# Kernel tuning notes

Measured on AMD Instinct MI355X. Metric: run time of the kernel, lower is better.

Reference implementation:

```python
import jax, jax.numpy as jnp
import numpy as np

D_MODEL = 1024
B, T = 4, 2048
LN_EPS = 1e-5


def setup_inputs() -> dict:
    key = jax.random.key(0)
    ks = jax.random.split(key, 8)
    d = D_MODEL
    x = jax.random.normal(ks[0], (B, T, d), dtype=jnp.float32)
    # linear params (fan-in scaled)
    W_in = jax.random.normal(ks[1], (d, 4 * d), dtype=jnp.float32) / np.sqrt(d)
    b_in = jnp.zeros((4 * d,), dtype=jnp.float32)
    W_out = jax.random.normal(ks[2], (2 * d, d), dtype=jnp.float32) / np.sqrt(2 * d)
    b_out = jnp.zeros((d,), dtype=jnp.float32)
    # LRU initializer (matches the torch module's initializer())
    rng = np.random.default_rng(0)
    r_min, r_max = 0.9, 0.999
    u1 = rng.random(d)
    u2 = rng.random(d)
    nu_log = np.log(-0.5 * np.log(u1 * (r_max ** 2 - r_min ** 2) + r_min ** 2))
    theta_log = np.log(u2 * np.pi * 2)
    gamma_log = np.log(np.sqrt(1 - np.exp(-np.exp(nu_log)) ** 2))
    # LayerNorm affine params
    ln_w = jnp.ones((2 * d,), dtype=jnp.float32)
    ln_b = jnp.zeros((2 * d,), dtype=jnp.float32)
    return {
        "x": x,
        "W_in": W_in, "b_in": b_in,
        "nu_log": jnp.asarray(nu_log, dtype=jnp.float32),
        "theta_log": jnp.asarray(theta_log, dtype=jnp.float32),
        "gamma_log": jnp.asarray(gamma_log, dtype=jnp.float32),
        "ln_w": ln_w, "ln_b": ln_b,
        "W_out": W_out, "b_out": b_out,
    }


def _complex_scan(in_r, in_i, f_r, f_i):
    """h_t = f * h_{t-1} + in_t over axis=1, complex math in real/imag pairs."""
    def combine(l, r):
        a1r, a1i, b1r, b1i = l
        a2r, a2i, b2r, b2i = r
        ar = a2r * a1r - a2i * a1i
        ai = a2r * a1i + a2i * a1r
        br = a2r * b1r - a2i * b1i + b2r
        bi = a2r * b1i + a2i * b1r + b2i
        return (ar, ai, br, bi)
    fr = jnp.broadcast_to(f_r, in_r.shape)
    fi = jnp.broadcast_to(f_i, in_i.shape)
    _, _, hr, hi = jax.lax.associative_scan(combine, (fr, fi, in_r, in_i), axis=1)
    return hr, hi


def reference(x, W_in, b_in, nu_log, theta_log, gamma_log, ln_w, ln_b, W_out, b_out):
    d = x.shape[-1]
    u = x @ W_in + b_in                       # [B, T, 4d]
    v, o = u[..., :2 * d], u[..., 2 * d:]     # each [B, T, 2d]
    nu = jnp.exp(-jnp.exp(nu_log))            # [d]
    theta = jnp.exp(theta_log)
    gamma = jnpp_exp = jnp.exp(gamma_log)
    f_r = nu * jnp.cos(theta)
    f_i = nu * jnp.sin(theta)
    in_r = gamma * v[..., :d]                 # [B, T, d]
    in_i = gamma * v[..., d:]
    h_r, h_i = _complex_scan(in_r, in_i, f_r, f_i)
    y = jnp.concatenate([h_r, h_i], axis=-1) * jax.nn.silu(o)  # [B, T, 2d]
    mu = jnp.mean(y, axis=-1, keepdims=True)
    var = jnp.mean(jnp.square(y - mu), axis=-1, keepdims=True)
    y = (y - mu) * jax.lax.rsqrt(var + LN_EPS) * ln_w + ln_b
    return y @ W_out + b_out                  # [B, T, d]
```

## Files before the change

### kernel.cpp

```cpp
#include <hip/hip_runtime.h>
#include <hip/hip_bf16.h>

#define D_MODEL 1024
#define BB 4
#define TT 2048
#define ROWS (BB*TT)
#define NCHUNK 64
#define CHLEN 32

typedef __attribute__((ext_vector_type(8))) short short8;
typedef __attribute__((ext_vector_type(4))) float floatx4;

static __device__ __forceinline__ ushort f2bf(float f) {
    union { float f; unsigned u; } v; v.f = f;
    unsigned r = v.u + 0x7FFF + ((v.u >> 16) & 1);
    return (ushort)(r >> 16);
}
static __device__ __forceinline__ float bf2f(ushort b) {
    union { unsigned u; float f; } v; v.u = ((unsigned)b) << 16;
    return v.f;
}

#define GLOAD_LDS16(gp, lp)                                                 \
    __builtin_amdgcn_global_load_lds(                                       \
        (const __attribute__((address_space(1))) void*)(gp),                \
        (__attribute__((address_space(3))) void*)(lp), 16, 0, 0)

#define PREP_A 8192
#define PREP_B 4096
#define PREP_C 2048
__global__ __launch_bounds__(256) void prep_all(
    const float* __restrict__ x, ushort* __restrict__ xb,
    const float* __restrict__ W_in, ushort* __restrict__ WinT,
    const float* __restrict__ W_out, ushort* __restrict__ W1T,
    const float* __restrict__ lnw, const float* __restrict__ lnb,
    float* __restrict__ s1, float* __restrict__ c2,
    const float* __restrict__ nu_log, const float* __restrict__ theta_log,
    const float* __restrict__ gamma_log,
    float* __restrict__ fr, float* __restrict__ fi, float* __restrict__ gm) {
    __shared__ float smem[32 * 33 + 8 * 32 * 2];
    int bid = blockIdx.x, tid = threadIdx.x;
    if (bid < PREP_A) {
        int i = bid * 256 + tid;
        float4 v = ((const float4*)x)[i];
        ushort4 o;
        o.x = f2bf(v.x); o.y = f2bf(v.y); o.z = f2bf(v.z); o.w = f2bf(v.w);
        ((ushort4*)xb)[i] = o;
    } else if (bid < PREP_A + PREP_B) {
        int b2 = bid - PREP_A;
        int n0 = (b2 & 127) * 32, k0 = (b2 >> 7) * 32;
        int tx = tid & 31, ty = tid >> 5;
        float (*tile)[33] = (float (*)[33])smem;
#pragma unroll
        for (int j = 0; j < 4; ++j)
            tile[ty + j*8][tx] = W_in[(size_t)(k0 + ty + j*8) * 4096 + n0 + tx];
        __syncthreads();
#pragma unroll
        for (int j = 0; j < 4; ++j)
            WinT[(size_t)(n0 + ty + j*8) * 1024 + k0 + tx] = f2bf(tile[tx][ty + j*8]);
    } else if (bid < PREP_A + PREP_B + PREP_C) {
        int b2 = bid - PREP_A - PREP_B;
        int n0 = (b2 & 31) * 32, k0 = (b2 >> 5) * 32;
        int tx = tid & 31, ty = tid >> 5;
        float (*tile)[33] = (float (*)[33])smem;
        float* red1 = smem + 32 * 33;
        float* red2 = red1 + 8 * 32;
        float p1 = 0.f, p2 = 0.f;
#pragma unroll
        for (int j = 0; j < 4; ++j) {
            int k = k0 + ty + j * 8;
            float w = W_out[(size_t)k * 1024 + n0 + tx];
            float lw = lnw[k], lb = lnb[k];
            tile[ty + j*8][tx] = lw * w;
            p1 += lw * w; p2 += lb * w;
        }
        __syncthreads();
#pragma unroll
        for (int j = 0; j < 4; ++j)
            W1T[(size_t)(n0 + ty + j*8) * 2048 + k0 + tx] = f2bf(tile[tx][ty + j*8]);
        red1[ty * 32 + tx] = p1; red2[ty * 32 + tx] = p2;
        __syncthreads();
        if (ty == 0) {
            float a = 0.f, b = 0.f;
#pragma unroll
            for (int t = 0; t < 8; ++t) { a += red1[t * 32 + tx]; b += red2[t * 32 + tx]; }
            atomicAdd(&s1[n0 + tx], a);
            atomicAdd(&c2[n0 + tx], b);
        }
    } else {
        int c = (bid - PREP_A - PREP_B - PREP_C) * 256 + tid;
        if (c < D_MODEL) {
            float nu = expf(-expf(nu_log[c]));
            float th = expf(theta_log[c]);
            fr[c] = nu * cosf(th);
            fi[c] = nu * sinf(th);
            gm[c] = expf(gamma_log[c]);
        }
    }
}

#define P_PRE  do { __builtin_amdgcn_sched_barrier(0); __builtin_amdgcn_s_barrier();  \
                    asm volatile("s_waitcnt lgkmcnt(0)" ::: "memory");                \
                    __builtin_amdgcn_sched_barrier(0);                                \
                    __builtin_amdgcn_s_setprio(1); } while (0)
#define P_POST do { __builtin_amdgcn_s_setprio(0); __builtin_amdgcn_sched_barrier(0); \
                    __builtin_amdgcn_s_barrier();                                     \
                    __builtin_amdgcn_sched_barrier(0); } while (0)

__global__ __launch_bounds__(512) void gemm256(
    const ushort* __restrict__ A, const ushort* __restrict__ B,
    int K, const float* __restrict__ bias,
    const float* __restrict__ gamma,
    ushort* __restrict__ out_r, ushort* __restrict__ out_i,
    ushort* __restrict__ out_o) {
    __shared__ ushort LA[2][256 * 64];
    __shared__ ushort LB[2][256 * 64];
    int tid = threadIdx.x;
    int lane = tid & 63;
    int wave = tid >> 6;
    int wp = wave >> 2;
    int wq = wave & 3;
    int lr = lane & 15, q = lane >> 4;
    int swl = lr & 7;
    int rs8 = tid >> 3, ch = tid & 7;
    int sw8 = (ch ^ (rs8 & 7)) * 8;

    int gx = gridDim.x;
    int nwg = gx * gridDim.y;
    int lid = blockIdx.y * gx + blockIdx.x;
    int per = nwg >> 3;
    int sid = (lid & 7) * per + (lid >> 3);
    long m0 = (long)(sid / gx) * 256;
    long n0 = (long)(sid % gx) * 256;
    const int NT = K >> 6;

    const ushort* Abase = A + (size_t)(m0 + rs8) * K + sw8;
    const ushort* Bbase = B + (size_t)(n0 + rs8) * K + sw8;

    floatx4 acc[8][4] = {};

#define STG_A(kt, P, R) GLOAD_LDS16(Abase + (size_t)(R) * K + (kt), \
                                    &LA[P][((R) + rs8) * 64 + ch * 8])
#define STG_B(kt, P, R) GLOAD_LDS16(Bbase + (size_t)(R) * K + (kt), \
                                    &LB[P][((R) + rs8) * 64 + ch * 8])

    STG_A(0, 0, 0);    STG_A(0, 0, 64);
    STG_B(0, 0, 0);    STG_B(0, 0, 64);
    STG_B(0, 0, 128);  STG_B(0, 0, 192);
    STG_A(0, 0, 128);  STG_A(0, 0, 192);
    STG_A(64, 1, 0);   STG_A(64, 1, 64);
    STG_B(64, 1, 0);   STG_B(64, 1, 64);
    STG_B(64, 1, 128); STG_B(64, 1, 192);
    asm volatile("s_waitcnt vmcnt(6)" ::: "memory");
    __builtin_amdgcn_s_barrier();

    for (int t = 0; t < NT; ++t) {
        const int p = t & 1;
        int kt1 = (t + 1 < NT) ? (t + 1) << 6 : 0;
        int kt2 = (t + 2 < NT) ? (t + 2) << 6 : 0;
        short8 a[2][4], b0[2][2], b1[2][2];

#pragma unroll
        for (int ks = 0; ks < 2; ++ks) {
#pragma unroll
            for (int r = 0; r < 4; ++r)
                a[ks][r] = *(const short8*)&LA[p][(wp * 64 + r * 16 + lr) * 64 + ((ks * 4 + q) ^ swl) * 8];
#pragma unroll
            for (int c = 0; c < 2; ++c)
                b0[ks][c] = *(const short8*)&LB[p][(wq * 32 + c * 16 + lr) * 64 + ((ks * 4 + q) ^ swl) * 8];
        }
        STG_A(kt1, p ^ 1, 128); STG_A(kt1, p ^ 1, 192);
        P_PRE;
#pragma unroll
        for (int ks = 0; ks < 2; ++ks)
#pragma unroll
            for (int r = 0; r < 4; ++r)
#pragma unroll
                for (int c = 0; c < 2; ++c)
                    acc[r][c] = __builtin_amdgcn_mfma_f32_16x16x32_bf16(
                        a[ks][r], b0[ks][c], acc[r][c], 0, 0, 0);
        P_POST;

#pragma unroll
        for (int ks = 0; ks < 2; ++ks)
#pragma unroll
            for (int c = 0; c < 2; ++c)
                b1[ks][c] = *(const short8*)&LB[p][(128 + wq * 32 + c * 16 + lr) * 64 + ((ks * 4 + q) ^ swl) * 8];
        STG_A(kt2, p, 0); STG_A(kt2, p, 64);
        P_PRE;
#pragma unroll
        for (int ks = 0; ks < 2; ++ks)
#pragma unroll
            for (int r = 0; r < 4; ++r)
#pragma unroll
                for (int c = 0; c < 2; ++c)
                    acc[r][2 + c] = __builtin_amdgcn_mfma_f32_16x16x32_bf16(
                        a[ks][r], b1[ks][c], acc[r][2 + c], 0, 0, 0);
        P_POST;

#pragma unroll
        for (int ks = 0; ks < 2; ++ks)
#pragma unroll
            for (int r = 0; r < 4; ++r)
                a[ks][r] = *(const short8*)&LA[p][(128 + wp * 64 + r * 16 + lr) * 64 + ((ks * 4 + q) ^ swl) * 8];
        STG_B(kt2, p, 0); STG_B(kt2, p, 64);
        P_PRE;
#pragma unroll
        for (int ks = 0; ks < 2; ++ks)
#pragma unroll
            for (int r = 0; r < 4; ++r)
#pragma unroll
                for (int c = 0; c < 2; ++c)
                    acc[4 + r][c] = __builtin_amdgcn_mfma_f32_16x16x32_bf16(
                        a[ks][r], b0[ks][c], acc[4 + r][c], 0, 0, 0);
        P_POST;

        STG_B(kt2, p, 128); STG_B(kt2, p, 192);
        asm volatile("s_waitcnt vmcnt(6)" ::: "memory");
        P_PRE;
#pragma unroll
        for (int ks = 0; ks < 2; ++ks)
#pragma unroll
            for (int r = 0; r < 4; ++r)
#pragma unroll
                for (int c = 0; c < 2; ++c)
                    acc[4 + r][2 + c] = __builtin_amdgcn_mfma_f32_16x16x32_bf16(
                        a[ks][r], b1[ks][c], acc[4 + r][2 + c], 0, 0, 0);
        P_POST;
    }
    asm volatile("s_waitcnt vmcnt(0)" ::: "memory");

    int sector = (int)(n0 >> 10);
    if (sector < 2) {
        ushort* dst = sector ? out_i : out_r;
#pragma unroll
        for (int nh = 0; nh < 2; ++nh)
#pragma unroll
            for (int c = 0; c < 2; ++c) {
                int lc = (int)(n0 & 1023) + nh * 128 + wq * 32 + c * 16 + lr;
                float bv = bias[(sector << 10) + lc];
                float gv = gamma[lc];
#pragma unroll
                for (int mh = 0; mh < 2; ++mh)
#pragma unroll
                    for (int r = 0; r < 4; ++r)
#pragma unroll
                        for (int g = 0; g < 4; ++g) {
                            long row = m0 + mh * 128 + wp * 64 + r * 16 + q * 4 + g;
                            dst[row * 1024 + lc] = f2bf(gv * (acc[mh * 4 + r][nh * 2 + c][g] + bv));
                        }
            }
    } else {
        int oc0 = (int)(n0 - 2048);
#pragma unroll
        for (int nh = 0; nh < 2; ++nh)
#pragma unroll
            for (int c = 0; c < 2; ++c) {
                int oc = oc0 + nh * 128 + wq * 32 + c * 16 + lr;
                float bv = bias[2048 + oc];
#pragma unroll
                for (int mh = 0; mh < 2; ++mh)
#pragma unroll
                    for (int r = 0; r < 4; ++r)
#pragma unroll
                        for (int g = 0; g < 4; ++g) {
                            long row = m0 + mh * 128 + wp * 64 + r * 16 + q * 4 + g;
                            out_o[row * 2048 + oc] = f2bf(acc[mh * 4 + r][nh * 2 + c][g] + bv);
                        }
            }
    }
#undef STG_A
#undef STG_B
}

__global__ __launch_bounds__(512) void gemm2_8ph(
    const ushort* __restrict__ A, const ushort* __restrict__ B,
    int K, int N, const float* __restrict__ bias, float* __restrict__ outC,
    const float* __restrict__ mu, const float* __restrict__ rs,
    const float* __restrict__ s1, const float* __restrict__ c2) {
    __shared__ ushort LA[2][128 * 64];
    __shared__ ushort LB[2][256 * 64];
    int tid = threadIdx.x;
    int lane = tid & 63;
    int wave = tid >> 6;
    int wp = wave >> 2;
    int wq = wave & 3;
    int lr = lane & 15, q = lane >> 4;
    int swl = lr & 7;
    int rs8 = tid >> 3, ch = tid & 7;
    int sw8 = (ch ^ (rs8 & 7)) * 8;

    int gx = gridDim.x;
    int nwg = gx * gridDim.y;
    int lid = blockIdx.y * gx + blockIdx.x;
    int per = nwg >> 3;
    int sid = (lid & 7) * per + (lid >> 3);
    long m0 = (long)(sid / gx) * 128;
    long n0 = (long)(sid % gx) * 256;
    const int NT = K >> 6;

    const ushort* Abase = A + (size_t)(m0 + rs8) * K + sw8;
    const ushort* Bbase = B + (size_t)(n0 + rs8) * K + sw8;

    floatx4 acc[4][4] = {};

#define STG2_A(kt, P, R) GLOAD_LDS16(Abase + (size_t)(R) * K + (kt), \
                                     &LA[P][((R) + rs8) * 64 + ch * 8])
#define STG2_B(kt, P, R) GLOAD_LDS16(Bbase + (size_t)(R) * K + (kt), \
                                     &LB[P][((R) + rs8) * 64 + ch * 8])

    STG2_A(0, 0, 0);   STG2_A(0, 0, 64);
    STG2_B(0, 0, 0);   STG2_B(0, 0, 64);
    STG2_B(0, 0, 128); STG2_B(0, 0, 192);
    STG2_A(64, 1, 0);
    STG2_B(64, 1, 0);  STG2_B(64, 1, 64);
    asm volatile("s_waitcnt vmcnt(3)" ::: "memory");
    __builtin_amdgcn_s_barrier();

    for (int t = 0; t < NT; ++t) {
        const int p = t & 1;
        int kt1 = (t + 1 < NT) ? (t + 1) << 6 : 0;
        int kt2 = (t + 2 < NT) ? (t + 2) << 6 : 0;
        short8 a[2][2], b0[2][2], b1[2][2];

#pragma unroll
        for (int ks = 0; ks < 2; ++ks) {
#pragma unroll
            for (int r = 0; r < 2; ++r)
                a[ks][r] = *(const short8*)&LA[p][(wp * 32 + r * 16 + lr) * 64 + ((ks * 4 + q) ^ swl) * 8];
#pragma unroll
            for (int c = 0; c < 2; ++c)
                b0[ks][c] = *(const short8*)&LB[p][(wq * 32 + c * 16 + lr) * 64 + ((ks * 4 + q) ^ swl) * 8];
        }
        STG2_A(kt1, p ^ 1, 64);
        STG2_B(kt1, p ^ 1, 128); STG2_B(kt1, p ^ 1, 192);
        P_PRE;
#pragma unroll
        for (int ks = 0; ks < 2; ++ks)
#pragma unroll
            for (int r = 0; r < 2; ++r)
#pragma unroll
                for (int c = 0; c < 2; ++c)
                    acc[r][c] = __builtin_amdgcn_mfma_f32_16x16x32_bf16(
                        a[ks][r], b0[ks][c], acc[r][c], 0, 0, 0);
        P_POST;

#pragma unroll
        for (int ks = 0; ks < 2; ++ks)
#pragma unroll
            for (int c = 0; c < 2; ++c)
                b1[ks][c] = *(const short8*)&LB[p][(128 + wq * 32 + c * 16 + lr) * 64 + ((ks * 4 + q) ^ swl) * 8];
        P_PRE;
#pragma unroll
        for (int ks = 0; ks < 2; ++ks)
#pragma unroll
            for (int r = 0; r < 2; ++r)
#pragma unroll
                for (int c = 0; c < 2; ++c)
                    acc[r][2 + c] = __builtin_amdgcn_mfma_f32_16x16x32_bf16(
                        a[ks][r], b1[ks][c], acc[r][2 + c], 0, 0, 0);
        P_POST;

#pragma unroll
        for (int ks = 0; ks < 2; ++ks)
#pragma unroll
            for (int r = 0; r < 2; ++r)
                a[ks][r] = *(const short8*)&LA[p][(64 + wp * 32 + r * 16 + lr) * 64 + ((ks * 4 + q) ^ swl) * 8];
        STG2_A(kt2, p, 0);
        P_PRE;
#pragma unroll
        for (int ks = 0; ks < 2; ++ks)
#pragma unroll
            for (int r = 0; r < 2; ++r)
#pragma unroll
                for (int c = 0; c < 2; ++c)
                    acc[2 + r][c] = __builtin_amdgcn_mfma_f32_16x16x32_bf16(
                        a[ks][r], b0[ks][c], acc[2 + r][c], 0, 0, 0);
        P_POST;

        STG2_B(kt2, p, 0); STG2_B(kt2, p, 64);
        asm volatile("s_waitcnt vmcnt(3)" ::: "memory");
        P_PRE;
#pragma unroll
        for (int ks = 0; ks < 2; ++ks)
#pragma unroll
            for (int r = 0; r < 2; ++r)
#pragma unroll
                for (int c = 0; c < 2; ++c)
                    acc[2 + r][2 + c] = __builtin_amdgcn_mfma_f32_16x16x32_bf16(
                        a[ks][r], b1[ks][c], acc[2 + r][2 + c], 0, 0, 0);
        P_POST;
    }
    asm volatile("s_waitcnt vmcnt(0)" ::: "memory");

#pragma unroll
    for (int nh = 0; nh < 2; ++nh)
#pragma unroll
        for (int c = 0; c < 2; ++c) {
            long col = n0 + nh * 128 + wq * 32 + c * 16 + lr;
            float bc = c2[col] + bias[col];
            float s1c = s1[col];
#pragma unroll
            for (int mh = 0; mh < 2; ++mh)
#pragma unroll
                for (int r = 0; r < 2; ++r)
#pragma unroll
                    for (int g = 0; g < 4; ++g) {
                        long row = m0 + mh * 64 + wp * 32 + r * 16 + q * 4 + g;
                        outC[row * (long)N + col] =
                            rs[row] * (acc[mh * 2 + r][nh * 2 + c][g] - mu[row] * s1c) + bc;
                    }
        }
#undef STG2_A
#undef STG2_B
}

__global__ __launch_bounds__(256) void scan_carries(
    const ushort* __restrict__ in_r, const ushort* __restrict__ in_i,
    float* __restrict__ carry,
    const float* __restrict__ fr_, const float* __restrict__ fi_) {
    int t = blockIdx.x * 256 + threadIdx.x;
    int cp = t & 511;
    int ck = (t >> 9) & (NCHUNK - 1);
    int b = t >> 15;
    int c0 = cp * 2;
    float f0r = fr_[c0], f0i = fi_[c0], f1r = fr_[c0 + 1], f1i = fi_[c0 + 1];
    size_t base = ((size_t)(b * TT + ck * CHLEN)) * 1024 + c0;
    float h0r = 0.f, h0i = 0.f, h1r = 0.f, h1i = 0.f;
#pragma unroll 8
    for (int j = 0; j < CHLEN; ++j) {
        uint ur = *(const uint*)(in_r + base + (size_t)j * 1024);
        uint ui = *(const uint*)(in_i + base + (size_t)j * 1024);
        float r0 = bf2f((ushort)ur), r1 = bf2f((ushort)(ur >> 16));
        float i0 = bf2f((ushort)ui), i1 = bf2f((ushort)(ui >> 16));
        float n0r = f0r * h0r - f0i * h0i + r0;
        float n0i = f0r * h0i + f0i * h0r + i0;
        float n1r = f1r * h1r - f1i * h1i + r1;
        float n1i = f1r * h1i + f1i * h1r + i1;
        h0r = n0r; h0i = n0i; h1r = n1r; h1i = n1i;
    }
    ((float4*)carry)[((size_t)b * NCHUNK + ck) * 512 + cp] =
        make_float4(h0r, h0i, h1r, h1i);
}

__global__ __launch_bounds__(256) void carry_prefix(
    float* __restrict__ carry,
    const float* __restrict__ fr_, const float* __restrict__ fi_) {
    int t = blockIdx.x * 256 + threadIdx.x;
    int cp = t & 511, b = t >> 9;
    int c0 = cp * 2;
    float a0r = fr_[c0], a0i = fi_[c0], a1r = fr_[c0 + 1], a1i = fi_[c0 + 1];
#pragma unroll
    for (int s = 0; s < 5; ++s) {
        float t0r = a0r * a0r - a0i * a0i, t0i = 2.f * a0r * a0i;
        float t1r = a1r * a1r - a1i * a1i, t1i = 2.f * a1r * a1i;
        a0r = t0r; a0i = t0i; a1r = t1r; a1i = t1i;
    }
    float4* base = (float4*)carry + (size_t)b * NCHUNK * 512 + cp;
    float C0r = 0.f, C0i = 0.f, C1r = 0.f, C1i = 0.f;
    for (int k = 0; k < NCHUNK; ++k) {
        float4 s = base[(size_t)k * 512];
        base[(size_t)k * 512] = make_float4(C0r, C0i, C1r, C1i);
        float n0r = a0r * C0r - a0i * C0i + s.x;
        float n0i = a0r * C0i + a0i * C0r + s.y;
        float n1r = a1r * C1r - a1i * C1i + s.z;
        float n1i = a1r * C1i + a1i * C1r + s.w;
        C0r = n0r; C0i = n0i; C1r = n1r; C1i = n1i;
    }
}

__global__ __launch_bounds__(256) void scan_apply(
    const ushort* __restrict__ in_r, const ushort* __restrict__ in_i,
    const float* __restrict__ carry,
    const float* __restrict__ fr_, const float* __restrict__ fi_,
    const ushort* __restrict__ o, ushort* __restrict__ yb) {
    int t = blockIdx.x * 256 + threadIdx.x;
    int cp = t & 511;
    int ck = (t >> 9) & (NCHUNK - 1);
    int b = t >> 15;
    int c0 = cp * 2;
    float f0r = fr_[c0], f0i = fi_[c0], f1r = fr_[c0 + 1], f1i = fi_[c0 + 1];
    float4 C = ((const float4*)carry)[((size_t)b * NCHUNK + ck) * 512 + cp];
    float h0r = C.x, h0i = C.y, h1r = C.z, h1i = C.w;
    size_t base = ((size_t)(b * TT + ck * CHLEN)) * 1024 + c0;
    size_t rowbase = (size_t)(b * TT + ck * CHLEN);
#pragma unroll 4
    for (int j = 0; j < CHLEN; ++j) {
        uint ur = *(const uint*)(in_r + base + (size_t)j * 1024);
        uint ui = *(const uint*)(in_i + base + (size_t)j * 1024);
        size_t ob = (rowbase + j) * 2048 + c0;
        uint uo1 = *(const uint*)(o + ob);
        uint uo2 = *(const uint*)(o + ob + 1024);
        float r0 = bf2f((ushort)ur), r1 = bf2f((ushort)(ur >> 16));
        float i0 = bf2f((ushort)ui), i1 = bf2f((ushort)(ui >> 16));
        float n0r = f0r * h0r - f0i * h0i + r0;
        float n0i = f0r * h0i + f0i * h0r + i0;
        float n1r = f1r * h1r - f1i * h1i + r1;
        float n1i = f1r * h1i + f1i * h1r + i1;
        h0r = n0r; h0i = n0i; h1r = n1r; h1i = n1i;
        float o00 = bf2f((ushort)uo1), o01 = bf2f((ushort)(uo1 >> 16));
        float o10 = bf2f((ushort)uo2), o11 = bf2f((ushort)(uo2 >> 16));
        float y00 = h0r * o00 / (1.f + __expf(-o00));
        float y01 = h1r * o01 / (1.f + __expf(-o01));
        float y10 = h0i * o10 / (1.f + __expf(-o10));
        float y11 = h1i * o11 / (1.f + __expf(-o11));
        *(uint*)(yb + ob) = (uint)f2bf(y00) | ((uint)f2bf(y01) << 16);
        *(uint*)(yb + ob + 1024) = (uint)f2bf(y10) | ((uint)f2bf(y11) << 16);
    }
}

__global__ __launch_bounds__(256) void row_stats(
    const ushort* __restrict__ yb, float* __restrict__ mu_o,
    float* __restrict__ rs_o) {
    long row = blockIdx.x;
    int tid = threadIdx.x;
    const ushort* p = yb + row * 2048 + tid * 8;
    uint4 raw = *(const uint4*)p;
    float s = 0.f, s2 = 0.f;
    unsigned w[4] = {raw.x, raw.y, raw.z, raw.w};
#pragma unroll
    for (int j = 0; j < 4; ++j) {
        float a = bf2f((ushort)(w[j] & 0xffff));
        float b = bf2f((ushort)(w[j] >> 16));
        s += a + b; s2 += a * a + b * b;
    }
#pragma unroll
    for (int off = 32; off > 0; off >>= 1) {
        s += __shfl_down(s, off, 64);
        s2 += __shfl_down(s2, off, 64);
    }
    __shared__ float red[8];
    int wv = tid >> 6;
    if ((tid & 63) == 0) { red[wv] = s; red[4 + wv] = s2; }
    __syncthreads();
    if (tid == 0) {
        s = red[0] + red[1] + red[2] + red[3];
        s2 = red[4] + red[5] + red[6] + red[7];
        float mu = s * (1.f / 2048.f);
        float var = s2 * (1.f / 2048.f) - mu * mu;
        mu_o[row] = mu;
        rs_o[row] = rsqrtf(var + 1e-5f);
    }
}


extern "C" void kernel_launch(void* const* d_in, const int* in_sizes, int n_in,
                              void* d_out, int out_size, void* d_ws, size_t ws_size,
                              hipStream_t stream) {
    const float* x         = (const float*)d_in[0];
    const float* W_in      = (const float*)d_in[1];
    const float* b_in      = (const float*)d_in[2];
    const float* nu_log    = (const float*)d_in[3];
    const float* theta_log = (const float*)d_in[4];
    const float* gamma_log = (const float*)d_in[5];
    const float* ln_w      = (const float*)d_in[6];
    const float* ln_b      = (const float*)d_in[7];
    const float* W_out     = (const float*)d_in[8];
    const float* b_out     = (const float*)d_in[9];
    float* out = (float*)d_out;

    char* ws = (char*)d_ws;
    size_t off = 0;
    auto alloc = [&](size_t bytes) {
        char* p = ws + off;
        off += (bytes + 255) & ~(size_t)255;
        return p;
    };
    ushort* xb    = (ushort*)alloc((size_t)ROWS * 1024 * 2);
    ushort* WinT  = (ushort*)alloc((size_t)4096 * 1024 * 2);
    ushort* W1T   = (ushort*)alloc((size_t)1024 * 2048 * 2);
    float*  fr    = (float*)alloc(1024 * 4);
    float*  fi    = (float*)alloc(1024 * 4);
    float*  gm    = (float*)alloc(1024 * 4);
    float*  s1c2  = (float*)alloc(2048 * 4);
    float*  s1    = s1c2;
    float*  c2    = s1c2 + 1024;
    ushort* in_r  = (ushort*)alloc((size_t)ROWS * 1024 * 2);
    ushort* in_i  = (ushort*)alloc((size_t)ROWS * 1024 * 2);
    ushort* obuf  = (ushort*)alloc((size_t)ROWS * 2048 * 2);
    float*  carry = (float*)alloc((size_t)BB * 1024 * NCHUNK * 2 * 4);
    ushort* yb    = (ushort*)alloc((size_t)ROWS * 2048 * 2);
    float*  muv   = (float*)alloc(ROWS * 4);
    float*  rsv   = (float*)alloc(ROWS * 4);

    hipMemsetAsync(s1c2, 0, 2048 * 4, stream);

    prep_all<<<PREP_A + PREP_B + PREP_C + 4, 256, 0, stream>>>(
        x, xb, W_in, WinT, W_out, W1T, ln_w, ln_b, s1, c2,
        nu_log, theta_log, gamma_log, fr, fi, gm);

    gemm256<<<dim3(4096 / 256, ROWS / 256), 512, 0, stream>>>(
        xb, WinT, 1024, b_in, gm, in_r, in_i, obuf);

    scan_carries<<<BB * 512 * NCHUNK / 256, 256, 0, stream>>>(in_r, in_i, carry, fr, fi);
    carry_prefix<<<BB * 512 / 256, 256, 0, stream>>>(carry, fr, fi);
    scan_apply<<<BB * 512 * NCHUNK / 256, 256, 0, stream>>>(
        in_r, in_i, carry, fr, fi, obuf, yb);

    row_stats<<<ROWS, 256, 0, stream>>>(yb, muv, rsv);

    gemm2_8ph<<<dim3(1024 / 256, ROWS / 128), 512, 0, stream>>>(
        yb, W1T, 2048, 1024, b_out, out, muv, rsv, s1, c2);
}
```

Measured before the change: 273.8 us.

## Fuse carry prefix and row statistics into the scan apply kernel

Removes the separate carry_prefix and row_stats kernels. Each scan_apply2 block, one per (batch, chunk), recomputes its own carry prefix by serially combining all preceding chunk carries, then computes the per-row LayerNorm mean and rstd with wave shuffles and a shared-memory reduction while producing y. This saves two launches and a full re-read of yb, at the cost of redundant carry work in later chunks and a cross-wave reduction on every timestep.

```diff
diff --git a/kernel.cpp b/kernel.cpp
--- a/kernel.cpp
+++ b/kernel.cpp
@@ -443,45 +443,38 @@
         make_float4(h0r, h0i, h1r, h1i);
 }
 
-__global__ __launch_bounds__(256) void carry_prefix(
-    float* __restrict__ carry,
-    const float* __restrict__ fr_, const float* __restrict__ fi_) {
-    int t = blockIdx.x * 256 + threadIdx.x;
-    int cp = t & 511, b = t >> 9;
+__global__ __launch_bounds__(512) void scan_apply2(
+    const ushort* __restrict__ in_r, const ushort* __restrict__ in_i,
+    const float* __restrict__ carry,
+    const float* __restrict__ fr_, const float* __restrict__ fi_,
+    const ushort* __restrict__ o, ushort* __restrict__ yb,
+    float* __restrict__ mu_o, float* __restrict__ rs_o) {
+    int bid = blockIdx.x;
+    int b = bid >> 6, ck = bid & (NCHUNK - 1);
+    int cp = threadIdx.x;
+    int wave = cp >> 6, lane = cp & 63;
     int c0 = cp * 2;
-    float a0r = fr_[c0], a0i = fi_[c0], a1r = fr_[c0 + 1], a1i = fi_[c0 + 1];
+    float f0r = fr_[c0], f0i = fi_[c0], f1r = fr_[c0 + 1], f1i = fi_[c0 + 1];
+
+    float a0r = f0r, a0i = f0i, a1r = f1r, a1i = f1i;
 #pragma unroll
     for (int s = 0; s < 5; ++s) {
         float t0r = a0r * a0r - a0i * a0i, t0i = 2.f * a0r * a0i;
         float t1r = a1r * a1r - a1i * a1i, t1i = 2.f * a1r * a1i;
         a0r = t0r; a0i = t0i; a1r = t1r; a1i = t1i;
     }
-    float4* base = (float4*)carry + (size_t)b * NCHUNK * 512 + cp;
-    float C0r = 0.f, C0i = 0.f, C1r = 0.f, C1i = 0.f;
-    for (int k = 0; k < NCHUNK; ++k) {
-        float4 s = base[(size_t)k * 512];
-        base[(size_t)k * 512] = make_float4(C0r, C0i, C1r, C1i);
-        float n0r = a0r * C0r - a0i * C0i + s.x;
-        float n0i = a0r * C0i + a0i * C0r + s.y;
-        float n1r = a1r * C1r - a1i * C1i + s.z;
-        float n1i = a1r * C1i + a1i * C1r + s.w;
-        C0r = n0r; C0i = n0i; C1r = n1r; C1i = n1i;
-    }
-}
-
-__global__ __launch_bounds__(256) void scan_apply(
-    const ushort* __restrict__ in_r, const ushort* __restrict__ in_i,
-    const float* __restrict__ carry,
-    const float* __restrict__ fr_, const float* __restrict__ fi_,
-    const ushort* __restrict__ o, ushort* __restrict__ yb) {
-    int t = blockIdx.x * 256 + threadIdx.x;
-    int cp = t & 511;
-    int ck = (t >> 9) & (NCHUNK - 1);
-    int b = t >> 15;
-    int c0 = cp * 2;
-    float f0r = fr_[c0], f0i = fi_[c0], f1r = fr_[c0 + 1], f1i = fi_[c0 + 1];
-    float4 C = ((const float4*)carry)[((size_t)b * NCHUNK + ck) * 512 + cp];
-    float h0r = C.x, h0i = C.y, h1r = C.z, h1i = C.w;
+    const float4* cb = (const float4*)carry + (size_t)b * NCHUNK * 512 + cp;
+    float h0r = 0.f, h0i = 0.f, h1r = 0.f, h1i = 0.f;
+    for (int k = 0; k < ck; ++k) {
+        float4 s = cb[(size_t)k * 512];
+        float n0r = a0r * h0r - a0i * h0i + s.x;
+        float n0i = a0r * h0i + a0i * h0r + s.y;
+        float n1r = a1r * h1r - a1i * h1i + s.z;
+        float n1i = a1r * h1i + a1i * h1r + s.w;
+        h0r = n0r; h0i = n0i; h1r = n1r; h1i = n1i;
+    }
+
+    __shared__ float sred[2][8][CHLEN];
     size_t base = ((size_t)(b * TT + ck * CHLEN)) * 1024 + c0;
     size_t rowbase = (size_t)(b * TT + ck * CHLEN);
 #pragma unroll 4
@@ -506,40 +499,24 @@
         float y11 = h1i * o11 / (1.f + __expf(-o11));
         *(uint*)(yb + ob) = (uint)f2bf(y00) | ((uint)f2bf(y01) << 16);
         *(uint*)(yb + ob + 1024) = (uint)f2bf(y10) | ((uint)f2bf(y11) << 16);
-    }
-}
-
-__global__ __launch_bounds__(256) void row_stats(
-    const ushort* __restrict__ yb, float* __restrict__ mu_o,
-    float* __restrict__ rs_o) {
-    long row = blockIdx.x;
-    int tid = threadIdx.x;
-    const ushort* p = yb + row * 2048 + tid * 8;
-    uint4 raw = *(const uint4*)p;
-    float s = 0.f, s2 = 0.f;
-    unsigned w[4] = {raw.x, raw.y, raw.z, raw.w};
-#pragma unroll
-    for (int j = 0; j < 4; ++j) {
-        float a = bf2f((ushort)(w[j] & 0xffff));
-        float b = bf2f((ushort)(w[j] >> 16));
-        s += a + b; s2 += a * a + b * b;
-    }
-#pragma unroll
-    for (int off = 32; off > 0; off >>= 1) {
-        s += __shfl_down(s, off, 64);
-        s2 += __shfl_down(s2, off, 64);
-    }
-    __shared__ float red[8];
-    int wv = tid >> 6;
-    if ((tid & 63) == 0) { red[wv] = s; red[4 + wv] = s2; }
+        float sp = y00 + y01 + y10 + y11;
+        float s2p = y00 * y00 + y01 * y01 + y10 * y10 + y11 * y11;
+#pragma unroll
+        for (int off = 32; off > 0; off >>= 1) {
+            sp += __shfl_xor(sp, off, 64);
+            s2p += __shfl_xor(s2p, off, 64);
+        }
+        if (lane == 0) { sred[0][wave][j] = sp; sred[1][wave][j] = s2p; }
+    }
     __syncthreads();
-    if (tid == 0) {
-        s = red[0] + red[1] + red[2] + red[3];
-        s2 = red[4] + red[5] + red[6] + red[7];
+    if (cp < CHLEN) {
+        float s = 0.f, s2 = 0.f;
+#pragma unroll
+        for (int w = 0; w < 8; ++w) { s += sred[0][w][cp]; s2 += sred[1][w][cp]; }
         float mu = s * (1.f / 2048.f);
         float var = s2 * (1.f / 2048.f) - mu * mu;
-        mu_o[row] = mu;
-        rs_o[row] = rsqrtf(var + 1e-5f);
+        mu_o[rowbase + cp] = mu;
+        rs_o[rowbase + cp] = rsqrtf(var + 1e-5f);
     }
 }
 
@@ -578,7 +555,7 @@
     ushort* in_r  = (ushort*)alloc((size_t)ROWS * 1024 * 2);
     ushort* in_i  = (ushort*)alloc((size_t)ROWS * 1024 * 2);
     ushort* obuf  = (ushort*)alloc((size_t)ROWS * 2048 * 2);
-    float*  carry = (float*)alloc((size_t)BB * 1024 * NCHUNK * 2 * 4);
+    float*  carry = (float*)alloc((size_t)BB * 512 * NCHUNK * 4 * 4);
     ushort* yb    = (ushort*)alloc((size_t)ROWS * 2048 * 2);
     float*  muv   = (float*)alloc(ROWS * 4);
     float*  rsv   = (float*)alloc(ROWS * 4);
@@ -593,11 +570,9 @@
         xb, WinT, 1024, b_in, gm, in_r, in_i, obuf);
 
     scan_carries<<<BB * 512 * NCHUNK / 256, 256, 0, stream>>>(in_r, in_i, carry, fr, fi);
-    carry_prefix<<<BB * 512 / 256, 256, 0, stream>>>(carry, fr, fi);
-    scan_apply<<<BB * 512 * NCHUNK / 256, 256, 0, stream>>>(
-        in_r, in_i, carry, fr, fi, obuf, yb);
-
-    row_stats<<<ROWS, 256, 0, stream>>>(yb, muv, rsv);
+
+    scan_apply2<<<BB * NCHUNK, 512, 0, stream>>>(
+        in_r, in_i, carry, fr, fi, obuf, yb, muv, rsv);
 
     gemm2_8ph<<<dim3(1024 / 256, ROWS / 128), 512, 0, stream>>>(
         yb, W1T, 2048, 1024, b_out, out, muv, rsv, s1, c2);
```

After: 284.3 us. +3.9%, slower.

## Restructure second GEMM main loop into a two-tile double-buffered schedule

Applied to the files above, without the earlier changes.

Replaces the 8-phase fine-grained interleaved prefetch schedule in the output GEMM with a simpler scheme. Each iteration now handles two K-tiles, and whole tiles are staged into the alternate LDS buffer while the current one is consumed. All B fragments are loaded up front and the global loads are fully drained with vmcnt(0) at each half-step. This cuts scheduling complexity, but the prefetch distance drops to one tile and the wait is full, so load latency may be less hidden than before. It also raises register pressure from holding b0 and b1 together.

```diff
diff --git a/kernel.cpp b/kernel.cpp
--- a/kernel.cpp
+++ b/kernel.cpp
@@ -273,7 +273,7 @@
 #undef STG_B
 }
 
-__global__ __launch_bounds__(512) void gemm2_8ph(
+__global__ __launch_bounds__(512) void gemm2_2t(
     const ushort* __restrict__ A, const ushort* __restrict__ B,
     int K, int N, const float* __restrict__ bias, float* __restrict__ outC,
     const float* __restrict__ mu, const float* __restrict__ rs,
@@ -298,6 +298,7 @@
     long m0 = (long)(sid / gx) * 128;
     long n0 = (long)(sid % gx) * 256;
     const int NT = K >> 6;
+    const int NI = NT >> 1;
 
     const ushort* Abase = A + (size_t)(m0 + rs8) * K + sw8;
     const ushort* Bbase = B + (size_t)(n0 + rs8) * K + sw8;
@@ -308,87 +309,110 @@
                                      &LA[P][((R) + rs8) * 64 + ch * 8])
 #define STG2_B(kt, P, R) GLOAD_LDS16(Bbase + (size_t)(R) * K + (kt), \
                                      &LB[P][((R) + rs8) * 64 + ch * 8])
-
-    STG2_A(0, 0, 0);   STG2_A(0, 0, 64);
-    STG2_B(0, 0, 0);   STG2_B(0, 0, 64);
-    STG2_B(0, 0, 128); STG2_B(0, 0, 192);
-    STG2_A(64, 1, 0);
-    STG2_B(64, 1, 0);  STG2_B(64, 1, 64);
-    asm volatile("s_waitcnt vmcnt(3)" ::: "memory");
+#define STG2_TILE(kt, P) do { STG2_A(kt, P, 0); STG2_A(kt, P, 64);            \
+                              STG2_B(kt, P, 0); STG2_B(kt, P, 64);            \
+                              STG2_B(kt, P, 128); STG2_B(kt, P, 192); } while (0)
+
+    STG2_TILE(0, 0);
+    asm volatile("s_waitcnt vmcnt(0)" ::: "memory");
     __builtin_amdgcn_s_barrier();
 
-    for (int t = 0; t < NT; ++t) {
-        const int p = t & 1;
-        int kt1 = (t + 1 < NT) ? (t + 1) << 6 : 0;
-        int kt2 = (t + 2 < NT) ? (t + 2) << 6 : 0;
+    for (int i = 0; i < NI; ++i) {
+        int t0 = 2 * i;
+        int kt1 = (t0 + 1) << 6;
+        int kt2 = (t0 + 2 < NT) ? (t0 + 2) << 6 : 0;
         short8 a[2][2], b0[2][2], b1[2][2];
 
 #pragma unroll
         for (int ks = 0; ks < 2; ++ks) {
 #pragma unroll
             for (int r = 0; r < 2; ++r)
-                a[ks][r] = *(const short8*)&LA[p][(wp * 32 + r * 16 + lr) * 64 + ((ks * 4 + q) ^ swl) * 8];
-#pragma unroll
-            for (int c = 0; c < 2; ++c)
-                b0[ks][c] = *(const short8*)&LB[p][(wq * 32 + c * 16 + lr) * 64 + ((ks * 4 + q) ^ swl) * 8];
+                a[ks][r] = *(const short8*)&LA[0][(wp * 32 + r * 16 + lr) * 64 + ((ks * 4 + q) ^ swl) * 8];
+#pragma unroll
+            for (int c = 0; c < 2; ++c) {
+                b0[ks][c] = *(const short8*)&LB[0][(wq * 32 + c * 16 + lr) * 64 + ((ks * 4 + q) ^ swl) * 8];
+                b1[ks][c] = *(const short8*)&LB[0][(128 + wq * 32 + c * 16 + lr) * 64 + ((ks * 4 + q) ^ swl) * 8];
+            }
         }
-        STG2_A(kt1, p ^ 1, 64);
-        STG2_B(kt1, p ^ 1, 128); STG2_B(kt1, p ^ 1, 192);
-        P_PRE;
-#pragma unroll
-        for (int ks = 0; ks < 2; ++ks)
-#pragma unroll
-            for (int r = 0; r < 2; ++r)
-#pragma unroll
-                for (int c = 0; c < 2; ++c)
+        STG2_TILE(kt1, 1);
+        P_PRE;
+#pragma unroll
+        for (int ks = 0; ks < 2; ++ks)
+#pragma unroll
+            for (int r = 0; r < 2; ++r)
+#pragma unroll
+                for (int c = 0; c < 2; ++c) {
                     acc[r][c] = __builtin_amdgcn_mfma_f32_16x16x32_bf16(
                         a[ks][r], b0[ks][c], acc[r][c], 0, 0, 0);
-        P_POST;
-
-#pragma unroll
-        for (int ks = 0; ks < 2; ++ks)
-#pragma unroll
-            for (int c = 0; c < 2; ++c)
-                b1[ks][c] = *(const short8*)&LB[p][(128 + wq * 32 + c * 16 + lr) * 64 + ((ks * 4 + q) ^ swl) * 8];
-        P_PRE;
-#pragma unroll
-        for (int ks = 0; ks < 2; ++ks)
-#pragma unroll
-            for (int r = 0; r < 2; ++r)
-#pragma unroll
-                for (int c = 0; c < 2; ++c)
                     acc[r][2 + c] = __builtin_amdgcn_mfma_f32_16x16x32_bf16(
                         a[ks][r], b1[ks][c], acc[r][2 + c], 0, 0, 0);
-        P_POST;
-
-#pragma unroll
-        for (int ks = 0; ks < 2; ++ks)
-#pragma unroll
-            for (int r = 0; r < 2; ++r)
-                a[ks][r] = *(const short8*)&LA[p][(64 + wp * 32 + r * 16 + lr) * 64 + ((ks * 4 + q) ^ swl) * 8];
-        STG2_A(kt2, p, 0);
-        P_PRE;
-#pragma unroll
-        for (int ks = 0; ks < 2; ++ks)
-#pragma unroll
-            for (int r = 0; r < 2; ++r)
-#pragma unroll
-                for (int c = 0; c < 2; ++c)
+                }
+        P_POST;
+
+#pragma unroll
+        for (int ks = 0; ks < 2; ++ks)
+#pragma unroll
+            for (int r = 0; r < 2; ++r)
+                a[ks][r] = *(const short8*)&LA[0][(64 + wp * 32 + r * 16 + lr) * 64 + ((ks * 4 + q) ^ swl) * 8];
+        P_PRE;
+#pragma unroll
+        for (int ks = 0; ks < 2; ++ks)
+#pragma unroll
+            for (int r = 0; r < 2; ++r)
+#pragma unroll
+                for (int c = 0; c < 2; ++c) {
                     acc[2 + r][c] = __builtin_amdgcn_mfma_f32_16x16x32_bf16(
                         a[ks][r], b0[ks][c], acc[2 + r][c], 0, 0, 0);
-        P_POST;
-
-        STG2_B(kt2, p, 0); STG2_B(kt2, p, 64);
-        asm volatile("s_waitcnt vmcnt(3)" ::: "memory");
-        P_PRE;
-#pragma unroll
-        for (int ks = 0; ks < 2; ++ks)
-#pragma unroll
-            for (int r = 0; r < 2; ++r)
-#pragma unroll
-                for (int c = 0; c < 2; ++c)
                     acc[2 + r][2 + c] = __builtin_amdgcn_mfma_f32_16x16x32_bf16(
                         a[ks][r], b1[ks][c], acc[2 + r][2 + c], 0, 0, 0);
+                }
+        asm volatile("s_waitcnt vmcnt(0)" ::: "memory");
+        P_POST;
+
+#pragma unroll
+        for (int ks = 0; ks < 2; ++ks) {
+#pragma unroll
+            for (int r = 0; r < 2; ++r)
+                a[ks][r] = *(const short8*)&LA[1][(wp * 32 + r * 16 + lr) * 64 + ((ks * 4 + q) ^ swl) * 8];
+#pragma unroll
+            for (int c = 0; c < 2; ++c) {
+                b0[ks][c] = *(const short8*)&LB[1][(wq * 32 + c * 16 + lr) * 64 + ((ks * 4 + q) ^ swl) * 8];
+                b1[ks][c] = *(const short8*)&LB[1][(128 + wq * 32 + c * 16 + lr) * 64 + ((ks * 4 + q) ^ swl) * 8];
+            }
+        }
+        STG2_TILE(kt2, 0);
+        P_PRE;
+#pragma unroll
+        for (int ks = 0; ks < 2; ++ks)
+#pragma unroll
+            for (int r = 0; r < 2; ++r)
+#pragma unroll
+                for (int c = 0; c < 2; ++c) {
+                    acc[r][c] = __builtin_amdgcn_mfma_f32_16x16x32_bf16(
+                        a[ks][r], b0[ks][c], acc[r][c], 0, 0, 0);
+                    acc[r][2 + c] = __builtin_amdgcn_mfma_f32_16x16x32_bf16(
+                        a[ks][r], b1[ks][c], acc[r][2 + c], 0, 0, 0);
+                }
+        P_POST;
+
+#pragma unroll
+        for (int ks = 0; ks < 2; ++ks)
+#pragma unroll
+            for (int r = 0; r < 2; ++r)
+                a[ks][r] = *(const short8*)&LA[1][(64 + wp * 32 + r * 16 + lr) * 64 + ((ks * 4 + q) ^ swl) * 8];
+        P_PRE;
+#pragma unroll
+        for (int ks = 0; ks < 2; ++ks)
+#pragma unroll
+            for (int r = 0; r < 2; ++r)
+#pragma unroll
+                for (int c = 0; c < 2; ++c) {
+                    acc[2 + r][c] = __builtin_amdgcn_mfma_f32_16x16x32_bf16(
+                        a[ks][r], b0[ks][c], acc[2 + r][c], 0, 0, 0);
+                    acc[2 + r][2 + c] = __builtin_amdgcn_mfma_f32_16x16x32_bf16(
+                        a[ks][r], b1[ks][c], acc[2 + r][2 + c], 0, 0, 0);
+                }
+        asm volatile("s_waitcnt vmcnt(0)" ::: "memory");
         P_POST;
     }
     asm volatile("s_waitcnt vmcnt(0)" ::: "memory");
@@ -413,6 +437,7 @@
         }
 #undef STG2_A
 #undef STG2_B
+#undef STG2_TILE
 }
 
 __global__ __launch_bounds__(256) void scan_carries(
@@ -599,6 +624,6 @@
 
     row_stats<<<ROWS, 256, 0, stream>>>(yb, muv, rsv);
 
-    gemm2_8ph<<<dim3(1024 / 256, ROWS / 128), 512, 0, stream>>>(
+    gemm2_2t<<<dim3(1024 / 256, ROWS / 128), 512, 0, stream>>>(
         yb, W1T, 2048, 1024, b_out, out, muv, rsv, s1, c2);
 }
```

Result: no change. 276.4 us (+0.9%).

## Widen scan kernels to four channels per thread, halve chunk length, one-wave row stats

Applied to the files above, without the earlier changes.

The chunked complex scan now has each thread handle four channels with 8-byte loads and stores, and uses 128 chunks of 16 steps instead of 64 of 32. This keeps the thread count the same while making memory accesses wider. The carry_prefix kernel now runs 1024 threads with a 128-step serial loop, which lengthens that serial phase. Row statistics now use one wavefront per row with four 16-byte loads per lane, which removes the shared-memory reduction and block sync.

```diff
diff --git a/kernel.cpp b/kernel.cpp
--- a/kernel.cpp
+++ b/kernel.cpp
@@ -5,8 +5,8 @@
 #define BB 4
 #define TT 2048
 #define ROWS (BB*TT)
-#define NCHUNK 64
-#define CHLEN 32
+#define NCHUNK 128
+#define CHLEN 16
 
 typedef __attribute__((ext_vector_type(8))) short short8;
 typedef __attribute__((ext_vector_type(4))) float floatx4;
@@ -420,52 +420,65 @@
     float* __restrict__ carry,
     const float* __restrict__ fr_, const float* __restrict__ fi_) {
     int t = blockIdx.x * 256 + threadIdx.x;
-    int cp = t & 511;
-    int ck = (t >> 9) & (NCHUNK - 1);
+    int cq = t & 255;
+    int ck = (t >> 8) & (NCHUNK - 1);
     int b = t >> 15;
-    int c0 = cp * 2;
-    float f0r = fr_[c0], f0i = fi_[c0], f1r = fr_[c0 + 1], f1i = fi_[c0 + 1];
+    int c0 = cq * 4;
+    float f_r[4], f_i[4], h_r[4] = {}, h_i[4] = {};
+#pragma unroll
+    for (int k = 0; k < 4; ++k) { f_r[k] = fr_[c0 + k]; f_i[k] = fi_[c0 + k]; }
     size_t base = ((size_t)(b * TT + ck * CHLEN)) * 1024 + c0;
-    float h0r = 0.f, h0i = 0.f, h1r = 0.f, h1i = 0.f;
-#pragma unroll 8
+#pragma unroll 4
     for (int j = 0; j < CHLEN; ++j) {
-        uint ur = *(const uint*)(in_r + base + (size_t)j * 1024);
-        uint ui = *(const uint*)(in_i + base + (size_t)j * 1024);
-        float r0 = bf2f((ushort)ur), r1 = bf2f((ushort)(ur >> 16));
-        float i0 = bf2f((ushort)ui), i1 = bf2f((ushort)(ui >> 16));
-        float n0r = f0r * h0r - f0i * h0i + r0;
-        float n0i = f0r * h0i + f0i * h0r + i0;
-        float n1r = f1r * h1r - f1i * h1i + r1;
-        float n1i = f1r * h1i + f1i * h1r + i1;
-        h0r = n0r; h0i = n0i; h1r = n1r; h1i = n1i;
-    }
-    ((float4*)carry)[((size_t)b * NCHUNK + ck) * 512 + cp] =
-        make_float4(h0r, h0i, h1r, h1i);
+        uint2 ur = *(const uint2*)(in_r + base + (size_t)j * 1024);
+        uint2 ui = *(const uint2*)(in_i + base + (size_t)j * 1024);
+        uint wr[2] = {ur.x, ur.y}, wi[2] = {ui.x, ui.y};
+#pragma unroll
+        for (int k = 0; k < 4; ++k) {
+            float r = bf2f((ushort)(wr[k >> 1] >> ((k & 1) * 16)));
+            float im = bf2f((ushort)(wi[k >> 1] >> ((k & 1) * 16)));
+            float nr = f_r[k] * h_r[k] - f_i[k] * h_i[k] + r;
+            float ni = f_r[k] * h_i[k] + f_i[k] * h_r[k] + im;
+            h_r[k] = nr; h_i[k] = ni;
+        }
+    }
+    float4* cw = (float4*)(carry + (((size_t)b * NCHUNK + ck) * 256 + cq) * 8);
+    cw[0] = make_float4(h_r[0], h_i[0], h_r[1], h_i[1]);
+    cw[1] = make_float4(h_r[2], h_i[2], h_r[3], h_i[3]);
 }
 
 __global__ __launch_bounds__(256) void carry_prefix(
     float* __restrict__ carry,
     const float* __restrict__ fr_, const float* __restrict__ fi_) {
     int t = blockIdx.x * 256 + threadIdx.x;
-    int cp = t & 511, b = t >> 9;
-    int c0 = cp * 2;
-    float a0r = fr_[c0], a0i = fi_[c0], a1r = fr_[c0 + 1], a1i = fi_[c0 + 1];
-#pragma unroll
-    for (int s = 0; s < 5; ++s) {
-        float t0r = a0r * a0r - a0i * a0i, t0i = 2.f * a0r * a0i;
-        float t1r = a1r * a1r - a1i * a1i, t1i = 2.f * a1r * a1i;
-        a0r = t0r; a0i = t0i; a1r = t1r; a1i = t1i;
-    }
-    float4* base = (float4*)carry + (size_t)b * NCHUNK * 512 + cp;
-    float C0r = 0.f, C0i = 0.f, C1r = 0.f, C1i = 0.f;
-    for (int k = 0; k < NCHUNK; ++k) {
-        float4 s = base[(size_t)k * 512];
-        base[(size_t)k * 512] = make_float4(C0r, C0i, C1r, C1i);
-        float n0r = a0r * C0r - a0i * C0i + s.x;
-        float n0i = a0r * C0i + a0i * C0r + s.y;
-        float n1r = a1r * C1r - a1i * C1i + s.z;
-        float n1i = a1r * C1i + a1i * C1r + s.w;
-        C0r = n0r; C0i = n0i; C1r = n1r; C1i = n1i;
+    int cq = t & 255, b = t >> 8;
+    int c0 = cq * 4;
+    float a_r[4], a_i[4], C_r[4] = {}, C_i[4] = {};
+#pragma unroll
+    for (int k = 0; k < 4; ++k) { a_r[k] = fr_[c0 + k]; a_i[k] = fi_[c0 + k]; }
+#pragma unroll
+    for (int s = 0; s < 4; ++s) {
+#pragma unroll
+        for (int k = 0; k < 4; ++k) {
+            float nr = a_r[k] * a_r[k] - a_i[k] * a_i[k];
+            float ni = 2.f * a_r[k] * a_i[k];
+            a_r[k] = nr; a_i[k] = ni;
+        }
+    }
+    float* base = carry + ((size_t)b * NCHUNK * 256 + cq) * 8;
+    for (int ckk = 0; ckk < NCHUNK; ++ckk) {
+        float4* p = (float4*)(base + (size_t)ckk * 256 * 8);
+        float4 s0 = p[0], s1v = p[1];
+        p[0] = make_float4(C_r[0], C_i[0], C_r[1], C_i[1]);
+        p[1] = make_float4(C_r[2], C_i[2], C_r[3], C_i[3]);
+        float sr[4] = {s0.x, s0.z, s1v.x, s1v.z};
+        float si[4] = {s0.y, s0.w, s1v.y, s1v.w};
+#pragma unroll
+        for (int k = 0; k < 4; ++k) {
+            float nr = a_r[k] * C_r[k] - a_i[k] * C_i[k] + sr[k];
+            float ni = a_r[k] * C_i[k] + a_i[k] * C_r[k] + si[k];
+            C_r[k] = nr; C_i[k] = ni;
+        }
     }
 }
 
@@ -475,67 +488,74 @@
     const float* __restrict__ fr_, const float* __restrict__ fi_,
     const ushort* __restrict__ o, ushort* __restrict__ yb) {
     int t = blockIdx.x * 256 + threadIdx.x;
-    int cp = t & 511;
-    int ck = (t >> 9) & (NCHUNK - 1);
+    int cq = t & 255;
+    int ck = (t >> 8) & (NCHUNK - 1);
     int b = t >> 15;
-    int c0 = cp * 2;
-    float f0r = fr_[c0], f0i = fi_[c0], f1r = fr_[c0 + 1], f1i = fi_[c0 + 1];
-    float4 C = ((const float4*)carry)[((size_t)b * NCHUNK + ck) * 512 + cp];
-    float h0r = C.x, h0i = C.y, h1r = C.z, h1i = C.w;
+    int c0 = cq * 4;
+    float f_r[4], f_i[4], h_r[4], h_i[4];
+#pragma unroll
+    for (int k = 0; k < 4; ++k) { f_r[k] = fr_[c0 + k]; f_i[k] = fi_[c0 + k]; }
+    const float4* cr = (const float4*)(carry + (((size_t)b * NCHUNK + ck) * 256 + cq) * 8);
+    float4 C0 = cr[0], C1 = cr[1];
+    h_r[0] = C0.x; h_i[0] = C0.y; h_r[1] = C0.z; h_i[1] = C0.w;
+    h_r[2] = C1.x; h_i[2] = C1.y; h_r[3] = C1.z; h_i[3] = C1.w;
     size_t base = ((size_t)(b * TT + ck * CHLEN)) * 1024 + c0;
     size_t rowbase = (size_t)(b * TT + ck * CHLEN);
 #pragma unroll 4
     for (int j = 0; j < CHLEN; ++j) {
-        uint ur = *(const uint*)(in_r + base + (size_t)j * 1024);
-        uint ui = *(const uint*)(in_i + base + (size_t)j * 1024);
+        uint2 ur = *(const uint2*)(in_r + base + (size_t)j * 1024);
+        uint2 ui = *(const uint2*)(in_i + base + (size_t)j * 1024);
         size_t ob = (rowbase + j) * 2048 + c0;
-        uint uo1 = *(const uint*)(o + ob);
-        uint uo2 = *(const uint*)(o + ob + 1024);
-        float r0 = bf2f((ushort)ur), r1 = bf2f((ushort)(ur >> 16));
-        float i0 = bf2f((ushort)ui), i1 = bf2f((ushort)(ui >> 16));
-        float n0r = f0r * h0r - f0i * h0i + r0;
-        float n0i = f0r * h0i + f0i * h0r + i0;
-        float n1r = f1r * h1r - f1i * h1i + r1;
-        float n1i = f1r * h1i + f1i * h1r + i1;
-        h0r = n0r; h0i = n0i; h1r = n1r; h1i = n1i;
-        float o00 = bf2f((ushort)uo1), o01 = bf2f((ushort)(uo1 >> 16));
-        float o10 = bf2f((ushort)uo2), o11 = bf2f((ushort)(uo2 >> 16));
-        float y00 = h0r * o00 / (1.f + __expf(-o00));
-        float y01 = h1r * o01 / (1.f + __expf(-o01));
-        float y10 = h0i * o10 / (1.f + __expf(-o10));
-        float y11 = h1i * o11 / (1.f + __expf(-o11));
-        *(uint*)(yb + ob) = (uint)f2bf(y00) | ((uint)f2bf(y01) << 16);
-        *(uint*)(yb + ob + 1024) = (uint)f2bf(y10) | ((uint)f2bf(y11) << 16);
+        uint2 uo1 = *(const uint2*)(o + ob);
+        uint2 uo2 = *(const uint2*)(o + ob + 1024);
+        uint wr[2] = {ur.x, ur.y}, wi[2] = {ui.x, ui.y};
+        uint w1[2] = {uo1.x, uo1.y}, w2[2] = {uo2.x, uo2.y};
+        uint y1[2], y2[2];
+#pragma unroll
+        for (int k = 0; k < 4; ++k) {
+            float r = bf2f((ushort)(wr[k >> 1] >> ((k & 1) * 16)));
+            float im = bf2f((ushort)(wi[k >> 1] >> ((k & 1) * 16)));
+            float nr = f_r[k] * h_r[k] - f_i[k] * h_i[k] + r;
+            float ni = f_r[k] * h_i[k] + f_i[k] * h_r[k] + im;
+            h_r[k] = nr; h_i[k] = ni;
+            float o1 = bf2f((ushort)(w1[k >> 1] >> ((k & 1) * 16)));
+            float o2 = bf2f((ushort)(w2[k >> 1] >> ((k & 1) * 16)));
+            float ya = h_r[k] * o1 / (1.f + __expf(-o1));
+            float ybv = h_i[k] * o2 / (1.f + __expf(-o2));
+            ushort pa = f2bf(ya), pb = f2bf(ybv);
+            if (k & 1) { y1[k >> 1] |= (uint)pa << 16; y2[k >> 1] |= (uint)pb << 16; }
+            else       { y1[k >> 1] = pa;              y2[k >> 1] = pb; }
+        }
+        *(uint2*)(yb + ob) = make_uint2(y1[0], y1[1]);
+        *(uint2*)(yb + ob + 1024) = make_uint2(y2[0], y2[1]);
     }
 }
 
 __global__ __launch_bounds__(256) void row_stats(
     const ushort* __restrict__ yb, float* __restrict__ mu_o,
     float* __restrict__ rs_o) {
-    long row = blockIdx.x;
     int tid = threadIdx.x;
-    const ushort* p = yb + row * 2048 + tid * 8;
-    uint4 raw = *(const uint4*)p;
+    long row = (long)blockIdx.x * 4 + (tid >> 6);
+    int lane = tid & 63;
+    const ushort* p = yb + row * 2048 + lane * 32;
     float s = 0.f, s2 = 0.f;
-    unsigned w[4] = {raw.x, raw.y, raw.z, raw.w};
 #pragma unroll
     for (int j = 0; j < 4; ++j) {
-        float a = bf2f((ushort)(w[j] & 0xffff));
-        float b = bf2f((ushort)(w[j] >> 16));
-        s += a + b; s2 += a * a + b * b;
+        uint4 raw = *(const uint4*)(p + j * 8);
+        unsigned w[4] = {raw.x, raw.y, raw.z, raw.w};
+#pragma unroll
+        for (int e = 0; e < 4; ++e) {
+            float a = bf2f((ushort)(w[e] & 0xffff));
+            float bq = bf2f((ushort)(w[e] >> 16));
+            s += a + bq; s2 += a * a + bq * bq;
+        }
     }
 #pragma unroll
     for (int off = 32; off > 0; off >>= 1) {
         s += __shfl_down(s, off, 64);
         s2 += __shfl_down(s2, off, 64);
     }
-    __shared__ float red[8];
-    int wv = tid >> 6;
-    if ((tid & 63) == 0) { red[wv] = s; red[4 + wv] = s2; }
-    __syncthreads();
-    if (tid == 0) {
-        s = red[0] + red[1] + red[2] + red[3];
-        s2 = red[4] + red[5] + red[6] + red[7];
+    if (lane == 0) {
         float mu = s * (1.f / 2048.f);
         float var = s2 * (1.f / 2048.f) - mu * mu;
         mu_o[row] = mu;
@@ -578,7 +598,7 @@
     ushort* in_r  = (ushort*)alloc((size_t)ROWS * 1024 * 2);
     ushort* in_i  = (ushort*)alloc((size_t)ROWS * 1024 * 2);
     ushort* obuf  = (ushort*)alloc((size_t)ROWS * 2048 * 2);
-    float*  carry = (float*)alloc((size_t)BB * 1024 * NCHUNK * 2 * 4);
+    float*  carry = (float*)alloc((size_t)BB * NCHUNK * 256 * 8 * 4);
     ushort* yb    = (ushort*)alloc((size_t)ROWS * 2048 * 2);
     float*  muv   = (float*)alloc(ROWS * 4);
     float*  rsv   = (float*)alloc(ROWS * 4);
@@ -592,12 +612,12 @@
     gemm256<<<dim3(4096 / 256, ROWS / 256), 512, 0, stream>>>(
         xb, WinT, 1024, b_in, gm, in_r, in_i, obuf);
 
-    scan_carries<<<BB * 512 * NCHUNK / 256, 256, 0, stream>>>(in_r, in_i, carry, fr, fi);
-    carry_prefix<<<BB * 512 / 256, 256, 0, stream>>>(carry, fr, fi);
-    scan_apply<<<BB * 512 * NCHUNK / 256, 256, 0, stream>>>(
+    scan_carries<<<BB * 256 * NCHUNK / 256, 256, 0, stream>>>(in_r, in_i, carry, fr, fi);
+    carry_prefix<<<BB * 256 / 256, 256, 0, stream>>>(carry, fr, fi);
+    scan_apply<<<BB * 256 * NCHUNK / 256, 256, 0, stream>>>(
         in_r, in_i, carry, fr, fi, obuf, yb);
 
-    row_stats<<<ROWS, 256, 0, stream>>>(yb, muv, rsv);
+    row_stats<<<ROWS / 4, 256, 0, stream>>>(yb, muv, rsv);
 
     gemm2_8ph<<<dim3(1024 / 256, ROWS / 128), 512, 0, stream>>>(
         yb, W1T, 2048, 1024, b_out, out, muv, rsv, s1, c2);
```

Measured after the change: 308.1 us. 1.13x slower.
